# Kernel tuning notes

Hardware: AMD Instinct MI355X
Metric: run time of the kernel (lower is better)

The kernel has to match this reference:

```python
import jax, jax.numpy as jnp
import numpy as np

TOP_K = 2  # matches init_kwargs top_k


def setup_inputs() -> dict:
    key = jax.random.key(0)
    ks = jax.random.split(key, 5)
    B, T, C, H, E = 4, 1024, 768, 3072, 8
    x = jax.random.normal(ks[0], (B, T, C), dtype=jnp.float32)
    Wg = jax.random.normal(ks[1], (C, E), dtype=jnp.float32) * 0.02
    W1 = jax.random.normal(ks[2], (E, C, H), dtype=jnp.float32) * (1.0 / np.sqrt(C))
    b1 = jnp.zeros((E, H), dtype=jnp.float32)
    W2 = jax.random.normal(ks[3], (E, H, C), dtype=jnp.float32) * (1.0 / np.sqrt(H))
    b2 = jnp.zeros((E, C), dtype=jnp.float32)
    return {"x": x, "Wg": Wg, "W1": W1, "b1": b1, "W2": W2, "b2": b2}


def reference(x, Wg, W1, b1, W2, b2):
    # TopKRouter: softmax over expert logits, keep top-k probs, zeros elsewhere.
    E = Wg.shape[-1]
    logits = jnp.einsum('btc,ce->bte', x, Wg)
    probs = jax.nn.softmax(logits, axis=-1)
    top_vals, top_idx = jax.lax.top_k(probs, TOP_K)          # (B,T,K)
    gates = (jax.nn.one_hot(top_idx, E, dtype=probs.dtype) * top_vals[..., None]).sum(-2)  # (B,T,E)

    # Per-expert FFN (Linear -> ReLU -> Linear; dropout is identity in eval),
    # combined with sparse gate weights (only top-k entries are nonzero).
    h = jax.nn.relu(jnp.einsum('btc,ech->bteh', x, W1) + b1)  # (B,T,E,H)
    y = jnp.einsum('bteh,ehc->btec', h, W2) + b2              # (B,T,E,C)
    out = jnp.einsum('bte,btec->btc', gates, y)               # (B,T,C)
    return out
```

## Files before the change

### kernel.cpp

```cpp
#include <hip/hip_runtime.h>
#include <hip/hip_bf16.h>
#include <cmath>

#define NT    4096
#define CDIM  768
#define HDIM  3072
#define NEXP  8
#define CAP   1280

typedef __bf16 bf16_t;
typedef __bf16 bf16x8 __attribute__((ext_vector_type(8)));
typedef float  f32x4  __attribute__((ext_vector_type(4)));

__device__ __forceinline__ void glds16(const void* g, void* l) {
    __builtin_amdgcn_global_load_lds(
        (const __attribute__((address_space(1))) void*)g,
        (__attribute__((address_space(3))) void*)l, 16, 0, 0);
}

__global__ __launch_bounds__(256)
void prep_kernel(const float* __restrict__ w1, const float* __restrict__ w2,
                 bf16_t* __restrict__ w1t, bf16_t* __restrict__ w2t) {
    __shared__ float tile[64][68];
    int z = blockIdx.z;
    bool isW1 = z < 8;
    int e = isW1 ? z : z - 8;
    int R  = isW1 ? CDIM : HDIM;
    int CC = isW1 ? HDIM : CDIM;
    const float* src = (isW1 ? w1 : w2) + (size_t)e * CDIM * HDIM;
    bf16_t* dst = (isW1 ? w1t : w2t) + (size_t)e * CDIM * HDIM;
    int ntc = CC / 64;
    int bx = blockIdx.x;
    int c0 = (bx % ntc) * 64, r0 = (bx / ntc) * 64;
    int t = threadIdx.x;
    int c4 = (t & 15) * 4, rr = t >> 4;
    #pragma unroll
    for (int i = 0; i < 4; i++) {
        int r = rr + i * 16;
        float4 v = *reinterpret_cast<const float4*>(&src[(size_t)(r0 + r) * CC + c0 + c4]);
        *reinterpret_cast<float4*>(&tile[r][c4]) = v;
    }
    __syncthreads();
    int r8 = (t & 7) * 8;
    #pragma unroll
    for (int i = 0; i < 2; i++) {
        int cc = (t >> 3) + i * 32;
        union { bf16_t h[8]; uint4 u; } pk;
        #pragma unroll
        for (int s = 0; s < 8; s++) pk.h[s] = (bf16_t)tile[r8 + s][cc];
        *reinterpret_cast<uint4*>(&dst[(size_t)(c0 + cc) * R + r0 + r8]) = pk.u;
    }
}

__global__ __launch_bounds__(256)
void router_kernel(const float* __restrict__ x, const float* __restrict__ wg,
                   bf16_t* __restrict__ xb,
                   int* __restrict__ counts, int* __restrict__ tmap,
                   float* __restrict__ gmap, int* __restrict__ smap) {
    __shared__ int lcnt[NEXP];
    __shared__ int gbase[NEXP];
    int tid = threadIdx.x, lane = tid & 63, wid = tid >> 6;
    if (tid < NEXP) lcnt[tid] = 0;
    __syncthreads();

    int ti0[4], ti1[4], tr0[4], tr1[4];
    float tg0[4], tg1[4];

    #pragma unroll
    for (int k = 0; k < 4; k++) {
        int t = blockIdx.x * 16 + wid * 4 + k;
        const float* xr = x + (size_t)t * CDIM;
        float acc[NEXP];
        #pragma unroll
        for (int e = 0; e < NEXP; e++) acc[e] = 0.f;
        #pragma unroll
        for (int i = 0; i < CDIM / 256; i++) {
            int c = (i * 64 + lane) * 4;
            float4 v = *reinterpret_cast<const float4*>(xr + c);
            union { bf16_t h[4]; uint2 u; } un;
            un.h[0] = (bf16_t)v.x; un.h[1] = (bf16_t)v.y;
            un.h[2] = (bf16_t)v.z; un.h[3] = (bf16_t)v.w;
            *reinterpret_cast<uint2*>(xb + (size_t)t * CDIM + c) = un.u;
            float vv[4] = {v.x, v.y, v.z, v.w};
            #pragma unroll
            for (int j = 0; j < 4; j++)
                #pragma unroll
                for (int e = 0; e < NEXP; e++)
                    acc[e] += vv[j] * wg[(c + j) * NEXP + e];
        }
        #pragma unroll
        for (int e = 0; e < NEXP; e++) {
            #pragma unroll
            for (int off = 32; off > 0; off >>= 1)
                acc[e] += __shfl_xor(acc[e], off, 64);
        }
        if (lane == 0) {
            float mx = acc[0];
            #pragma unroll
            for (int e = 1; e < NEXP; e++) mx = fmaxf(mx, acc[e]);
            float p[NEXP], s = 0.f;
            #pragma unroll
            for (int e = 0; e < NEXP; e++) { p[e] = expf(acc[e] - mx); s += p[e]; }
            float inv = 1.f / s;
            int i0 = 0;
            #pragma unroll
            for (int e = 1; e < NEXP; e++) if (p[e] > p[i0]) i0 = e;
            int i1 = (i0 == 0) ? 1 : 0;
            #pragma unroll
            for (int e = 0; e < NEXP; e++) if (e != i0 && p[e] > p[i1]) i1 = e;
            ti0[k] = i0; ti1[k] = i1;
            tg0[k] = p[i0] * inv; tg1[k] = p[i1] * inv;
            tr0[k] = atomicAdd(&lcnt[i0], 1);
            tr1[k] = atomicAdd(&lcnt[i1], 1);
        }
    }
    __syncthreads();
    if (tid < NEXP) gbase[tid] = atomicAdd(&counts[tid], lcnt[tid]);
    __syncthreads();
    if (lane == 0) {
        #pragma unroll
        for (int k = 0; k < 4; k++) {
            int t = blockIdx.x * 16 + wid * 4 + k;
            int c0 = gbase[ti0[k]] + tr0[k]; if (c0 >= CAP) c0 = CAP - 1;
            int c1 = gbase[ti1[k]] + tr1[k]; if (c1 >= CAP) c1 = CAP - 1;
            int s0 = ti0[k] * CAP + c0, s1 = ti1[k] * CAP + c1;
            tmap[s0] = t; gmap[s0] = tg0[k]; smap[t * 2]     = s0;
            tmap[s1] = t; gmap[s1] = tg1[k]; smap[t * 2 + 1] = s1;
        }
    }
}

__global__ __launch_bounds__(256)
void moe_gemm1_kernel(const bf16_t* __restrict__ xb, const bf16_t* __restrict__ w1t,
                      const float* __restrict__ b1, const int* __restrict__ counts,
                      const int* __restrict__ tmap, bf16_t* __restrict__ hws) {
    int h = blockIdx.x;
    int e = h & 7;
    int local = h >> 3;
    int mt = local / (HDIM / 128);
    int nt = local - mt * (HDIM / 128);
    int cnt = counts[e]; if (cnt > CAP) cnt = CAP;
    if (mt * 128 >= cnt) return;
    int m0 = e * CAP + mt * 128;
    int rend = e * CAP + cnt;
    int n0 = nt * 128;

    __shared__ __attribute__((aligned(16))) bf16_t As[128 * 32];
    __shared__ __attribute__((aligned(16))) bf16_t Bs[128 * 32];

    int tid = threadIdx.x, lane = tid & 63, wid = tid >> 6;
    const bf16_t* aP[2];
    const bf16_t* bP[2];
    int reg[2];
    #pragma unroll
    for (int it = 0; it < 2; it++) {
        int region = wid * 2 + it;
        int row = region * 16 + (lane >> 2);
        int kk = (lane & 3) * 8;
        int pos = m0 + row;
        if (pos > rend - 1) pos = rend - 1;
        aP[it] = xb + (size_t)tmap[pos] * CDIM + kk;
        bP[it] = w1t + ((size_t)e * HDIM + n0 + row) * CDIM + kk;
        reg[it] = region * 512;
    }

    int wm = (wid >> 1) * 64, wn = (wid & 1) * 64;
    int q = lane >> 4, mr = lane & 15;

    f32x4 acc[4][4];
    #pragma unroll
    for (int i = 0; i < 4; i++)
        #pragma unroll
        for (int j = 0; j < 4; j++)
            acc[i][j] = (f32x4){0.f, 0.f, 0.f, 0.f};

    for (int k0 = 0; k0 < CDIM; k0 += 32) {
        #pragma unroll
        for (int it = 0; it < 2; it++) {
            glds16(aP[it] + k0, As + reg[it]);
            glds16(bP[it] + k0, Bs + reg[it]);
        }
        __syncthreads();
        bf16x8 af[4], bfr[4];
        #pragma unroll
        for (int ti = 0; ti < 4; ti++)
            af[ti] = *reinterpret_cast<const bf16x8*>(&As[(wm + ti * 16 + mr) * 32 + q * 8]);
        #pragma unroll
        for (int tj = 0; tj < 4; tj++)
            bfr[tj] = *reinterpret_cast<const bf16x8*>(&Bs[(wn + tj * 16 + mr) * 32 + q * 8]);
        #pragma unroll
        for (int ti = 0; ti < 4; ti++)
            #pragma unroll
            for (int tj = 0; tj < 4; tj++)
                acc[ti][tj] = __builtin_amdgcn_mfma_f32_16x16x32_bf16(af[ti], bfr[tj], acc[ti][tj], 0, 0, 0);
        __syncthreads();
    }

    const float* be = b1 + (size_t)e * HDIM + n0;
    #pragma unroll
    for (int ti = 0; ti < 4; ti++) {
        #pragma unroll
        for (int r = 0; r < 4; r++) {
            int pos = m0 + wm + ti * 16 + q * 4 + r;
            if (pos < rend) {
                bf16_t* hrow = hws + (size_t)pos * HDIM + n0;
                #pragma unroll
                for (int tj = 0; tj < 4; tj++) {
                    float v = acc[ti][tj][r] + be[wn + tj * 16 + mr];
                    hrow[wn + tj * 16 + mr] = (bf16_t)fmaxf(v, 0.f);
                }
            }
        }
    }
}

__global__ __launch_bounds__(256)
void moe_gemm2_kernel(const bf16_t* __restrict__ hws, const bf16_t* __restrict__ w2t,
                      const float* __restrict__ b2, const int* __restrict__ counts,
                      const float* __restrict__ gmap, float* __restrict__ yws) {
    int h = blockIdx.x;
    int e = h & 7;
    int local = h >> 3;
    int mt = local / (CDIM / 128);
    int nt = local - mt * (CDIM / 128);
    int cnt = counts[e]; if (cnt > CAP) cnt = CAP;
    if (mt * 128 >= cnt) return;
    int m0 = e * CAP + mt * 128;
    int rend = e * CAP + cnt;
    int n0 = nt * 128;

    __shared__ __attribute__((aligned(16))) bf16_t As[128 * 32];
    __shared__ __attribute__((aligned(16))) bf16_t Bs[128 * 32];

    int tid = threadIdx.x, lane = tid & 63, wid = tid >> 6;
    const bf16_t* aP[2];
    const bf16_t* bP[2];
    int reg[2];
    #pragma unroll
    for (int it = 0; it < 2; it++) {
        int region = wid * 2 + it;
        int row = region * 16 + (lane >> 2);
        int kk = (lane & 3) * 8;
        int pos = m0 + row;
        if (pos > rend - 1) pos = rend - 1;
        aP[it] = hws + (size_t)pos * HDIM + kk;
        bP[it] = w2t + ((size_t)e * CDIM + n0 + row) * HDIM + kk;
        reg[it] = region * 512;
    }

    int wm = (wid >> 1) * 64, wn = (wid & 1) * 64;
    int q = lane >> 4, mr = lane & 15;

    f32x4 acc[4][4];
    #pragma unroll
    for (int i = 0; i < 4; i++)
        #pragma unroll
        for (int j = 0; j < 4; j++)
            acc[i][j] = (f32x4){0.f, 0.f, 0.f, 0.f};

    for (int k0 = 0; k0 < HDIM; k0 += 32) {
        #pragma unroll
        for (int it = 0; it < 2; it++) {
            glds16(aP[it] + k0, As + reg[it]);
            glds16(bP[it] + k0, Bs + reg[it]);
        }
        __syncthreads();
        bf16x8 af[4], bfr[4];
        #pragma unroll
        for (int ti = 0; ti < 4; ti++)
            af[ti] = *reinterpret_cast<const bf16x8*>(&As[(wm + ti * 16 + mr) * 32 + q * 8]);
        #pragma unroll
        for (int tj = 0; tj < 4; tj++)
            bfr[tj] = *reinterpret_cast<const bf16x8*>(&Bs[(wn + tj * 16 + mr) * 32 + q * 8]);
        #pragma unroll
        for (int ti = 0; ti < 4; ti++)
            #pragma unroll
            for (int tj = 0; tj < 4; tj++)
                acc[ti][tj] = __builtin_amdgcn_mfma_f32_16x16x32_bf16(af[ti], bfr[tj], acc[ti][tj], 0, 0, 0);
        __syncthreads();
    }

    const float* be = b2 + (size_t)e * CDIM + n0;
    #pragma unroll
    for (int ti = 0; ti < 4; ti++) {
        #pragma unroll
        for (int r = 0; r < 4; r++) {
            int pos = m0 + wm + ti * 16 + q * 4 + r;
            if (pos < rend) {
                float g = gmap[pos];
                float* yrow = yws + (size_t)pos * CDIM + n0;
                #pragma unroll
                for (int tj = 0; tj < 4; tj++) {
                    float v = acc[ti][tj][r] + be[wn + tj * 16 + mr];
                    yrow[wn + tj * 16 + mr] = g * v;
                }
            }
        }
    }
}

__global__ __launch_bounds__(256)
void combine_kernel(const float* __restrict__ yws, const int* __restrict__ smap,
                    float* __restrict__ out) {
    int idx = blockIdx.x * 256 + threadIdx.x;
    int t = idx / (CDIM / 4);
    int c = (idx - t * (CDIM / 4)) * 4;
    int s0 = smap[t * 2], s1 = smap[t * 2 + 1];
    float4 a = *reinterpret_cast<const float4*>(yws + (size_t)s0 * CDIM + c);
    float4 b = *reinterpret_cast<const float4*>(yws + (size_t)s1 * CDIM + c);
    float4 o = {a.x + b.x, a.y + b.y, a.z + b.z, a.w + b.w};
    *reinterpret_cast<float4*>(out + (size_t)t * CDIM + c) = o;
}

extern "C" void kernel_launch(void* const* d_in, const int* in_sizes, int n_in,
                              void* d_out, int out_size, void* d_ws, size_t ws_size,
                              hipStream_t stream) {
    const float* x  = (const float*)d_in[0];
    const float* wg = (const float*)d_in[1];
    const float* w1 = (const float*)d_in[2];
    const float* b1 = (const float*)d_in[3];
    const float* w2 = (const float*)d_in[4];
    const float* b2 = (const float*)d_in[5];
    float* out = (float*)d_out;

    char* w = (char*)d_ws;
    size_t off = 0;
    bf16_t* xb  = (bf16_t*)(w + off); off += (size_t)NT * CDIM * 2;
    bf16_t* w1t = (bf16_t*)(w + off); off += (size_t)NEXP * CDIM * HDIM * 2;
    bf16_t* w2t = (bf16_t*)(w + off); off += (size_t)NEXP * CDIM * HDIM * 2;
    bf16_t* hws = (bf16_t*)(w + off); off += (size_t)NEXP * CAP * HDIM * 2;
    float* yws  = (float*)w1t;
    int* counts = (int*)(w + off);  off += 64;
    int* tmap   = (int*)(w + off);  off += (size_t)NEXP * CAP * 4;
    int* smap   = (int*)(w + off);  off += (size_t)NT * 2 * 4;
    float* gmap = (float*)(w + off);

    hipMemsetAsync(counts, 0, NEXP * sizeof(int), stream);

    router_kernel<<<NT / 16, 256, 0, stream>>>(x, wg, xb, counts, tmap, gmap, smap);
    prep_kernel<<<dim3((CDIM / 64) * (HDIM / 64), 1, 16), 256, 0, stream>>>(
        w1, w2, w1t, w2t);

    moe_gemm1_kernel<<<8 * (CAP / 128) * (HDIM / 128), 256, 0, stream>>>(
        xb, w1t, b1, counts, tmap, hws);
    moe_gemm2_kernel<<<8 * (CAP / 128) * (CDIM / 128), 256, 0, stream>>>(
        hws, w2t, b2, counts, gmap, yws);
    combine_kernel<<<NT * (CDIM / 4) / 256, 256, 0, stream>>>(yws, smap, out);
}
```

Before: 357.8 us.

## Double K-tile depth to 64 and XOR-swizzle LDS layout in MoE GEMMs

Both expert GEMM kernels now stage 64-wide K slices per iteration instead of 32, halving the number of barrier pairs per output tile. The global-to-LDS loads write rows with an XOR swizzle on the 16-byte chunk index, and fragment reads apply the matching swizzle so that rows 128 bytes apart no longer collide on the same LDS banks. LDS use per block doubles to 32 KB, which may reduce occupancy, and loads still are not double-buffered.

Measured after the change: 345.3 us. 3.5% less time.

```diff
diff --git a/kernel.cpp b/kernel.cpp
--- a/kernel.cpp
+++ b/kernel.cpp
@@ -145,27 +145,29 @@
     int rend = e * CAP + cnt;
     int n0 = nt * 128;
 
-    __shared__ __attribute__((aligned(16))) bf16_t As[128 * 32];
-    __shared__ __attribute__((aligned(16))) bf16_t Bs[128 * 32];
+    __shared__ __attribute__((aligned(16))) bf16_t As[128 * 64];
+    __shared__ __attribute__((aligned(16))) bf16_t Bs[128 * 64];
 
     int tid = threadIdx.x, lane = tid & 63, wid = tid >> 6;
-    const bf16_t* aP[2];
-    const bf16_t* bP[2];
-    int reg[2];
-    #pragma unroll
-    for (int it = 0; it < 2; it++) {
-        int region = wid * 2 + it;
-        int row = region * 16 + (lane >> 2);
-        int kk = (lane & 3) * 8;
+    int rr = tid >> 3;
+    int pc = tid & 7;
+    int lc = pc ^ (rr & 7);
+    const bf16_t* aPj[4];
+    const bf16_t* bPj[4];
+    int ldsOff[4];
+    #pragma unroll
+    for (int j = 0; j < 4; j++) {
+        int row = j * 32 + rr;
         int pos = m0 + row;
         if (pos > rend - 1) pos = rend - 1;
-        aP[it] = xb + (size_t)tmap[pos] * CDIM + kk;
-        bP[it] = w1t + ((size_t)e * HDIM + n0 + row) * CDIM + kk;
-        reg[it] = region * 512;
+        aPj[j] = xb + (size_t)tmap[pos] * CDIM + lc * 8;
+        bPj[j] = w1t + ((size_t)e * HDIM + n0 + row) * CDIM + lc * 8;
+        ldsOff[j] = j * 2048 + wid * 512;
     }
 
     int wm = (wid >> 1) * 64, wn = (wid & 1) * 64;
     int q = lane >> 4, mr = lane & 15;
+    int sw = mr & 7;
 
     f32x4 acc[4][4];
     #pragma unroll
@@ -174,25 +176,29 @@
         for (int j = 0; j < 4; j++)
             acc[i][j] = (f32x4){0.f, 0.f, 0.f, 0.f};
 
-    for (int k0 = 0; k0 < CDIM; k0 += 32) {
-        #pragma unroll
-        for (int it = 0; it < 2; it++) {
-            glds16(aP[it] + k0, As + reg[it]);
-            glds16(bP[it] + k0, Bs + reg[it]);
+    for (int k0 = 0; k0 < CDIM; k0 += 64) {
+        #pragma unroll
+        for (int j = 0; j < 4; j++) {
+            glds16(aPj[j] + k0, As + ldsOff[j]);
+            glds16(bPj[j] + k0, Bs + ldsOff[j]);
         }
         __syncthreads();
-        bf16x8 af[4], bfr[4];
-        #pragma unroll
-        for (int ti = 0; ti < 4; ti++)
-            af[ti] = *reinterpret_cast<const bf16x8*>(&As[(wm + ti * 16 + mr) * 32 + q * 8]);
-        #pragma unroll
-        for (int tj = 0; tj < 4; tj++)
-            bfr[tj] = *reinterpret_cast<const bf16x8*>(&Bs[(wn + tj * 16 + mr) * 32 + q * 8]);
-        #pragma unroll
-        for (int ti = 0; ti < 4; ti++)
+        #pragma unroll
+        for (int ks = 0; ks < 2; ks++) {
+            int slot = ((ks * 4 + q) ^ sw) * 8;
+            bf16x8 af[4], bfr[4];
+            #pragma unroll
+            for (int ti = 0; ti < 4; ti++)
+                af[ti] = *reinterpret_cast<const bf16x8*>(&As[(wm + ti * 16 + mr) * 64 + slot]);
             #pragma unroll
             for (int tj = 0; tj < 4; tj++)
-                acc[ti][tj] = __builtin_amdgcn_mfma_f32_16x16x32_bf16(af[ti], bfr[tj], acc[ti][tj], 0, 0, 0);
+                bfr[tj] = *reinterpret_cast<const bf16x8*>(&Bs[(wn + tj * 16 + mr) * 64 + slot]);
+            #pragma unroll
+            for (int ti = 0; ti < 4; ti++)
+                #pragma unroll
+                for (int tj = 0; tj < 4; tj++)
+                    acc[ti][tj] = __builtin_amdgcn_mfma_f32_16x16x32_bf16(af[ti], bfr[tj], acc[ti][tj], 0, 0, 0);
+        }
         __syncthreads();
     }
 
@@ -229,27 +235,29 @@
     int rend = e * CAP + cnt;
     int n0 = nt * 128;
 
-    __shared__ __attribute__((aligned(16))) bf16_t As[128 * 32];
-    __shared__ __attribute__((aligned(16))) bf16_t Bs[128 * 32];
+    __shared__ __attribute__((aligned(16))) bf16_t As[128 * 64];
+    __shared__ __attribute__((aligned(16))) bf16_t Bs[128 * 64];
 
     int tid = threadIdx.x, lane = tid & 63, wid = tid >> 6;
-    const bf16_t* aP[2];
-    const bf16_t* bP[2];
-    int reg[2];
-    #pragma unroll
-    for (int it = 0; it < 2; it++) {
-        int region = wid * 2 + it;
-        int row = region * 16 + (lane >> 2);
-        int kk = (lane & 3) * 8;
+    int rr = tid >> 3;
+    int pc = tid & 7;
+    int lc = pc ^ (rr & 7);
+    const bf16_t* aPj[4];
+    const bf16_t* bPj[4];
+    int ldsOff[4];
+    #pragma unroll
+    for (int j = 0; j < 4; j++) {
+        int row = j * 32 + rr;
         int pos = m0 + row;
         if (pos > rend - 1) pos = rend - 1;
-        aP[it] = hws + (size_t)pos * HDIM + kk;
-        bP[it] = w2t + ((size_t)e * CDIM + n0 + row) * HDIM + kk;
-        reg[it] = region * 512;
+        aPj[j] = hws + (size_t)pos * HDIM + lc * 8;
+        bPj[j] = w2t + ((size_t)e * CDIM + n0 + row) * HDIM + lc * 8;
+        ldsOff[j] = j * 2048 + wid * 512;
     }
 
     int wm = (wid >> 1) * 64, wn = (wid & 1) * 64;
     int q = lane >> 4, mr = lane & 15;
+    int sw = mr & 7;
 
     f32x4 acc[4][4];
     #pragma unroll
@@ -258,25 +266,29 @@
         for (int j = 0; j < 4; j++)
             acc[i][j] = (f32x4){0.f, 0.f, 0.f, 0.f};
 
-    for (int k0 = 0; k0 < HDIM; k0 += 32) {
-        #pragma unroll
-        for (int it = 0; it < 2; it++) {
-            glds16(aP[it] + k0, As + reg[it]);
-            glds16(bP[it] + k0, Bs + reg[it]);
+    for (int k0 = 0; k0 < HDIM; k0 += 64) {
+        #pragma unroll
+        for (int j = 0; j < 4; j++) {
+            glds16(aPj[j] + k0, As + ldsOff[j]);
+            glds16(bPj[j] + k0, Bs + ldsOff[j]);
         }
         __syncthreads();
-        bf16x8 af[4], bfr[4];
-        #pragma unroll
-        for (int ti = 0; ti < 4; ti++)
-            af[ti] = *reinterpret_cast<const bf16x8*>(&As[(wm + ti * 16 + mr) * 32 + q * 8]);
-        #pragma unroll
-        for (int tj = 0; tj < 4; tj++)
-            bfr[tj] = *reinterpret_cast<const bf16x8*>(&Bs[(wn + tj * 16 + mr) * 32 + q * 8]);
-        #pragma unroll
-        for (int ti = 0; ti < 4; ti++)
+        #pragma unroll
+        for (int ks = 0; ks < 2; ks++) {
+            int slot = ((ks * 4 + q) ^ sw) * 8;
+            bf16x8 af[4], bfr[4];
+            #pragma unroll
+            for (int ti = 0; ti < 4; ti++)
+                af[ti] = *reinterpret_cast<const bf16x8*>(&As[(wm + ti * 16 + mr) * 64 + slot]);
             #pragma unroll
             for (int tj = 0; tj < 4; tj++)
-                acc[ti][tj] = __builtin_amdgcn_mfma_f32_16x16x32_bf16(af[ti], bfr[tj], acc[ti][tj], 0, 0, 0);
+                bfr[tj] = *reinterpret_cast<const bf16x8*>(&Bs[(wn + tj * 16 + mr) * 64 + slot]);
+            #pragma unroll
+            for (int ti = 0; ti < 4; ti++)
+                #pragma unroll
+                for (int tj = 0; tj < 4; tj++)
+                    acc[ti][tj] = __builtin_amdgcn_mfma_f32_16x16x32_bf16(af[ti], bfr[tj], acc[ti][tj], 0, 0, 0);
+        }
         __syncthreads();
     }
 
```
